# Kernel optimization log

Measured on AMD Instinct MI355X. Metric: run time of the kernel, lower is better.

The kernel has to match this reference:

```python
import jax, jax.numpy as jnp
import numpy as np

VOCAB = 32000
D_VEC = 1024

def setup_inputs() -> dict:
    key = jax.random.key(0)
    kq, ke = jax.random.split(key)
    q = jax.random.normal(kq, (4, 1024, D_VEC), dtype=jnp.float32)
    # emb_matrix ~ Uniform(-0.1, 0.1), as in torch .uniform_(-0.1, 0.1)
    emb_matrix = jax.random.uniform(ke, (VOCAB, D_VEC), dtype=jnp.float32,
                                    minval=-0.1, maxval=0.1)
    return {"q": q, "emb_matrix": emb_matrix}

def reference(q, emb_matrix):
    # scores: [B, L, V] = q @ emb^T  (unscaled single-head attention)
    scores = jnp.einsum('bld,vd->blv', q, emb_matrix)
    attn = jax.nn.softmax(scores, axis=-1)
    # dropout is identity in eval / deterministic reference
    ctx = jnp.einsum('blv,vd->bld', attn, emb_matrix)
    return ctx + q
```

## Files before the change

kernel.cpp:

```cpp
#include <hip/hip_runtime.h>
#include <hip/hip_bf16.h>

#define D_DIM 1024
#define VOCABSZ 32000
#define NROWSZ 4096
#define MBLK 64
#define LOG2E 1.44269504088896340736f

typedef unsigned short u16;
typedef short s8v __attribute__((ext_vector_type(8)));
typedef short s4v __attribute__((ext_vector_type(4)));
typedef float f4v __attribute__((ext_vector_type(4)));
typedef __attribute__((address_space(3))) const char* lds_p3;

static __device__ __forceinline__ u16 f2bf(float f) {
  union { float f; unsigned int u; } x; x.f = f;
  unsigned int r = x.u + 0x7fffu + ((x.u >> 16) & 1u);
  return (u16)(r >> 16);
}
static __device__ __forceinline__ unsigned int pack2(float lo, float hi) {
  return (unsigned int)f2bf(lo) | ((unsigned int)f2bf(hi) << 16);
}
static __device__ __forceinline__ unsigned int pk_rn(float lo, float hi) {
  float2 f; f.x = lo; f.y = hi;
  union { __hip_bfloat162 h; unsigned int u; } v;
  v.h = __float22bfloat162_rn(f);
  return v.u;
}
#define EXP2(x) __builtin_amdgcn_exp2f(x)

static __device__ __forceinline__ float bf2f(u16 b) {
  union { unsigned int u; float f; } x; x.u = ((unsigned int)b) << 16;
  return x.f;
}
static __device__ __forceinline__ float bfu_lo(unsigned int u) {
  union { unsigned int u; float f; } x; x.u = u << 16; return x.f;
}
static __device__ __forceinline__ float bfu_hi(unsigned int u) {
  union { unsigned int u; float f; } x; x.u = u & 0xffff0000u; return x.f;
}
static __device__ __forceinline__ f4v MFMA(s8v a, s8v b, f4v c) {
  return __builtin_amdgcn_mfma_f32_16x16x32_bf16(a, b, c, 0, 0, 0);
}

#define GLOAD_LDS16(gp, lp)                                                  \
  __builtin_amdgcn_global_load_lds(                                         \
      (const __attribute__((address_space(1))) void*)(gp),                  \
      (__attribute__((address_space(3))) void*)(lp), 16, 0, 0)

__global__ __launch_bounds__(256) void cvt3_kernel(const float* __restrict__ emb,
                                                   char* __restrict__ ETt) {
  const int b = blockIdx.x, t = threadIdx.x;
  const int v0 = b * 32;
  char* outp = ETt + ((size_t)b << 16);
#pragma unroll
  for (int k = 0; k < 16; ++k) {
    int ci = t + 256 * k;
    int v = ci >> 7;
    int d8 = ci & 127;
    const float* s = emb + (size_t)(v0 + v) * D_DIM + d8 * 8;
    float4 a = *(const float4*)s;
    float4 bb = *(const float4*)(s + 4);
    uint4 x;
    x.x = pack2(a.x, a.y); x.y = pack2(a.z, a.w);
    x.z = pack2(bb.x, bb.y); x.w = pack2(bb.z, bb.w);
    int off = ((v >> 2) * 64 + (d8 >> 1)) * 128 + (v & 3) * 32 + (d8 & 1) * 16;
    *(uint4*)(outp + off) = x;
  }
}

template <int NSPLIT>
__global__ __launch_bounds__(512, 2) void flash9_kernel(
    const float* __restrict__ qg, const char* __restrict__ ETt,
    float* __restrict__ out, u16* __restrict__ pctx, float* __restrict__ pstat) {
  __shared__ char ring[2 * 65536];
  __shared__ uint2 Sred[8 * 4 * 64];
  __shared__ char Plds[4096];
  __shared__ float lred[8][16];

  const int tid = threadIdx.x;
  const int w = tid >> 6;
  const int l = tid & 63;
  const int g = l >> 4;
  const int c = l & 15;
  const int ds = w & 3;
  const int mh = w >> 2;
  const int bid = blockIdx.x;
  const int sp = (NSPLIT == 4) ? (bid & 3) : 0;
  const int rb = (NSPLIT == 4) ? (bid >> 2) : bid;
  const int row0 = rb * MBLK;
  const int vslice = VOCABSZ / NSPLIT;
  const int ntiles = vslice / 32;
  const int gt0 = sp * ntiles;

  const f4v fzero = {0.f, 0.f, 0.f, 0.f};

  s8v qf[2][8];
#pragma unroll
  for (int mt = 0; mt < 2; ++mt)
#pragma unroll
    for (int kt = 0; kt < 8; ++kt) {
      const float* src = qg + (size_t)(row0 + mh * 32 + 16 * mt + c) * D_DIM +
                         ds * 256 + 32 * kt + 8 * g;
      float4 a = *(const float4*)src;
      float4 b = *(const float4*)(src + 4);
      s8v v;
      v[0] = (short)f2bf(a.x * LOG2E); v[1] = (short)f2bf(a.y * LOG2E);
      v[2] = (short)f2bf(a.z * LOG2E); v[3] = (short)f2bf(a.w * LOG2E);
      v[4] = (short)f2bf(b.x * LOG2E); v[5] = (short)f2bf(b.y * LOG2E);
      v[6] = (short)f2bf(b.z * LOG2E); v[7] = (short)f2bf(b.w * LOG2E);
      qf[mt][kt] = v;
    }

  f4v acc[2][16];
#pragma unroll
  for (int mt = 0; mt < 2; ++mt)
#pragma unroll
    for (int nt = 0; nt < 16; ++nt) acc[mt][nt] = fzero;

  float lcur = 0.f;

#define STAGE(U)                                                             \
  {                                                                          \
    const char* _gs = ETt + (((size_t)(gt0 + (U))) << 16) + tid * 16;        \
    char* _ls = ring + (((U) & 1) << 16) + tid * 16;                         \
    _Pragma("unroll") for (int _j = 0; _j < 8; ++_j)                         \
        GLOAD_LDS16(_gs + _j * 8192, _ls + _j * 8192);                       \
  }

  STAGE(0);
  __syncthreads();

  for (int t = 0; t < ntiles; ++t) {
    const char* buf = ring + ((t & 1) << 16);

#pragma unroll
    for (int vt = 0; vt < 2; ++vt) {
      const char* bp = buf + (((4 * vt + (c >> 2)) * 64 + 16 * ds + (g >> 1)) * 128 +
                              (c & 3) * 32 + (g & 1) * 16);
      f4v st0 = fzero, st1 = fzero;
#pragma unroll
      for (int kt = 0; kt < 8; ++kt) {
        s8v ek = *(const s8v*)(bp + kt * 256);
        st0 = MFMA(ek, qf[0][kt], st0);
        st1 = MFMA(ek, qf[1][kt], st1);
      }
      int qb = ((mh * 4 + vt * 2) * 4 + ds) * 64 + l;
      uint2 pk;
      pk.x = pk_rn(st0[0], st0[1]); pk.y = pk_rn(st0[2], st0[3]);
      Sred[qb] = pk;
      pk.x = pk_rn(st1[0], st1[1]); pk.y = pk_rn(st1[2], st1[3]);
      Sred[qb + 256] = pk;
    }
    __syncthreads();

    {
      int qq = mh * 4 + ds;
      f4v ss = fzero;
#pragma unroll
      for (int ww = 0; ww < 4; ++ww) {
        uint2 u = Sred[(qq * 4 + ww) * 64 + l];
        ss[0] += bfu_lo(u.x); ss[1] += bfu_hi(u.x);
        ss[2] += bfu_lo(u.y); ss[3] += bfu_hi(u.y);
      }
      float p0 = EXP2(ss[0]), p1 = EXP2(ss[1]);
      float p2 = EXP2(ss[2]), p3 = EXP2(ss[3]);
      int pb = mh * 2048 + (16 * (ds & 1) + c) * 64 + (16 * (ds >> 1) + 4 * g) * 2;
      uint2 pw; pw.x = pk_rn(p0, p1); pw.y = pk_rn(p2, p3);
      *(uint2*)(Plds + pb) = pw;
      lcur += (p0 + p1) + (p2 + p3);
    }
    __syncthreads();

    if (t + 1 < ntiles) STAGE(t + 1);

    {
      int pab = mh * 2048 + c * 64 + g * 16;
      s8v pa0 = *(const s8v*)(Plds + pab);
      s8v pa1 = *(const s8v*)(Plds + pab + 1024);
#pragma unroll
      for (int bb = 0; bb < 2; ++bb) {
        s4v trv[16];
#pragma unroll
        for (int k = 0; k < 8; ++k) {
          int nt = bb * 8 + k;
          const char* a0 = buf + ((2 * g) * 64 + 16 * ds + nt) * 128 + c * 2;
          asm volatile("ds_read_b64_tr_b16 %0, %1"
                       : "=v"(trv[2 * k]) : "v"((lds_p3)a0));
          asm volatile("ds_read_b64_tr_b16 %0, %1"
                       : "=v"(trv[2 * k + 1]) : "v"((lds_p3)(a0 + 8192)));
        }
        asm volatile("s_waitcnt lgkmcnt(0)" ::: "memory");
        __builtin_amdgcn_sched_barrier(0);
#pragma unroll
        for (int k = 0; k < 8; ++k) {
          int nt = bb * 8 + k;
          union { s4v s[2]; s8v v; } ev;
          ev.s[0] = trv[2 * k]; ev.s[1] = trv[2 * k + 1];
          acc[0][nt] = MFMA(pa0, ev.v, acc[0][nt]);
          acc[1][nt] = MFMA(pa1, ev.v, acc[1][nt]);
        }
      }
    }
  }
#undef STAGE

  {
    float lp = lcur;
    lp += __shfl_xor(lp, 16);
    lp += __shfl_xor(lp, 32);
    __syncthreads();
    if (g == 0) lred[mh * 4 + ds][c] = lp;
  }
  __syncthreads();

  if (NSPLIT == 1) {
#pragma unroll
    for (int mt = 0; mt < 2; ++mt) {
      float inv[4];
#pragma unroll
      for (int r = 0; r < 4; ++r)
        inv[r] = 1.f / (lred[mh * 4 + mt][4 * g + r] + lred[mh * 4 + 2 + mt][4 * g + r]);
#pragma unroll
      for (int nt = 0; nt < 16; ++nt)
#pragma unroll
        for (int r = 0; r < 4; ++r) {
          size_t o = (size_t)(row0 + mh * 32 + 16 * mt + 4 * g + r) * D_DIM +
                     ds * 256 + 16 * nt + c;
          out[o] = acc[mt][nt][r] * inv[r] + qg[o];
        }
    }
  } else {
    u16* pc = pctx + (size_t)sp * NROWSZ * D_DIM;
#pragma unroll
    for (int mt = 0; mt < 2; ++mt)
#pragma unroll
      for (int nt = 0; nt < 16; ++nt)
#pragma unroll
        for (int r = 0; r < 4; ++r)
          pc[(size_t)(row0 + mh * 32 + 16 * mt + 4 * g + r) * D_DIM +
             ds * 256 + 16 * nt + c] = f2bf(acc[mt][nt][r]);
    if (ds < 2 && g == 0)
      pstat[(size_t)sp * NROWSZ + row0 + mh * 32 + 16 * ds + c] =
          lred[mh * 4 + ds][c] + lred[mh * 4 + 2 + ds][c];
  }
}

__global__ __launch_bounds__(256) void combine2_kernel(const float* __restrict__ qg,
                                                       const u16* __restrict__ pctx,
                                                       const float* __restrict__ pstat,
                                                       float* __restrict__ out) {
  const int r = blockIdx.x;
  const int t = threadIdx.x;
  float L = pstat[r] + pstat[NROWSZ + r] + pstat[2 * NROWSZ + r] + pstat[3 * NROWSZ + r];
  float inv = 1.f / L;
  size_t o = (size_t)r * D_DIM + t * 4;
  float sx = 0.f, sy = 0.f, sz = 0.f, sw = 0.f;
#pragma unroll
  for (int sp = 0; sp < 4; ++sp) {
    ushort4 u = *(const ushort4*)(pctx + (size_t)sp * NROWSZ * D_DIM + o);
    sx += bf2f(u.x); sy += bf2f(u.y); sz += bf2f(u.z); sw += bf2f(u.w);
  }
  float4 qv = *(const float4*)(qg + o);
  float4 res;
  res.x = sx * inv + qv.x;
  res.y = sy * inv + qv.y;
  res.z = sz * inv + qv.z;
  res.w = sw * inv + qv.w;
  *(float4*)(out + o) = res;
}

__global__ __launch_bounds__(256) void naive_kernel(const float* __restrict__ qg,
                                                    const float* __restrict__ emb,
                                                    float* __restrict__ out) {
  __shared__ float s[VOCABSZ];
  __shared__ float qrow[D_DIM];
  __shared__ float lsh[4];
  const int r = blockIdx.x;
  const int t = threadIdx.x;
  for (int i = t; i < D_DIM; i += 256) qrow[i] = qg[(size_t)r * D_DIM + i];
  __syncthreads();
  float lpart = 0.f;
  for (int v = t; v < VOCABSZ; v += 256) {
    float dot = 0.f;
    for (int d = 0; d < D_DIM; d += 4) {
      float4 e = *(const float4*)(emb + (size_t)v * D_DIM + d);
      dot += qrow[d] * e.x + qrow[d + 1] * e.y + qrow[d + 2] * e.z + qrow[d + 3] * e.w;
    }
    float p = exp2f(dot * LOG2E);
    s[v] = p;
    lpart += p;
  }
  for (int o = 32; o; o >>= 1) lpart += __shfl_xor(lpart, o);
  if ((t & 63) == 0) lsh[t >> 6] = lpart;
  __syncthreads();
  float inv = 1.f / (lsh[0] + lsh[1] + lsh[2] + lsh[3]);
  float ax = 0.f, ay = 0.f, az = 0.f, aw = 0.f;
  for (int v = 0; v < VOCABSZ; ++v) {
    float p = s[v];
    float4 e = *(const float4*)(emb + (size_t)v * D_DIM + t * 4);
    ax += p * e.x; ay += p * e.y; az += p * e.z; aw += p * e.w;
  }
  size_t o = (size_t)r * D_DIM + t * 4;
  float4 qv = *(const float4*)(qg + o);
  float4 res;
  res.x = ax * inv + qv.x;
  res.y = ay * inv + qv.y;
  res.z = az * inv + qv.z;
  res.w = aw * inv + qv.w;
  *(float4*)(out + o) = res;
}

extern "C" void kernel_launch(void* const* d_in, const int* in_sizes, int n_in,
                              void* d_out, int out_size, void* d_ws, size_t ws_size,
                              hipStream_t stream) {
  const float* q = (const float*)d_in[0];
  const float* emb = (const float*)d_in[1];
  float* out = (float*)d_out;
  char* ws = (char*)d_ws;

  const size_t ETT_BYTES = 65536000ull;
  const size_t PCTX_BYTES = 4ull * NROWSZ * D_DIM * 2;
  const size_t PSTAT_BYTES = 4ull * NROWSZ * 4;

  if (ws_size >= ETT_BYTES + PCTX_BYTES + PSTAT_BYTES) {
    char* ETt = ws;
    u16* pctx = (u16*)(ws + ETT_BYTES);
    float* pstat = (float*)(ws + ETT_BYTES + PCTX_BYTES);
    cvt3_kernel<<<VOCABSZ / 32, 256, 0, stream>>>(emb, ETt);
    flash9_kernel<4><<<256, 512, 0, stream>>>(q, ETt, out, pctx, pstat);
    combine2_kernel<<<NROWSZ, 256, 0, stream>>>(q, pctx, pstat, out);
  } else if (ws_size >= ETT_BYTES) {
    char* ETt = ws;
    cvt3_kernel<<<VOCABSZ / 32, 256, 0, stream>>>(emb, ETt);
    flash9_kernel<1><<<NROWSZ / MBLK, 512, 0, stream>>>(q, ETt, out, nullptr, nullptr);
  } else {
    naive_kernel<<<NROWSZ, 256, 0, stream>>>(q, emb, out);
  }
}
```

Baseline: 591.0 us.

## Software-pipeline the P·V MFMAs across tiles to overlap them with the softmax exp phase

Splits each tile's P·V accumulation into four quarters. The first two quarters run right after the tile's probabilities are ready. The last two are deferred into the next iteration's softmax phase, where they are interleaved with the Sred reduction and exp2 work and issued at raised wave priority. The P buffer in LDS is double-buffered so the previous tile's probabilities stay readable, and a drain block after the loop finishes the final tile's deferred MFMAs. The goal is to hide the exp/reduction latency behind matrix work, at the cost of extra LDS, more register pressure from live transposed fragments, and more complex control flow.

```diff
diff --git a/kernel.cpp b/kernel.cpp
--- a/kernel.cpp
+++ b/kernel.cpp
@@ -42,6 +42,12 @@
 static __device__ __forceinline__ f4v MFMA(s8v a, s8v b, f4v c) {
   return __builtin_amdgcn_mfma_f32_16x16x32_bf16(a, b, c, 0, 0, 0);
 }
+
+#define LGKM0_SB()                                            \
+  do {                                                        \
+    asm volatile("s_waitcnt lgkmcnt(0)" ::: "memory");        \
+    __builtin_amdgcn_sched_barrier(0);                        \
+  } while (0)
 
 #define GLOAD_LDS16(gp, lp)                                                  \
   __builtin_amdgcn_global_load_lds(                                         \
@@ -70,12 +76,12 @@
 }
 
 template <int NSPLIT>
-__global__ __launch_bounds__(512, 2) void flash9_kernel(
+__global__ __launch_bounds__(512, 2) void flash11_kernel(
     const float* __restrict__ qg, const char* __restrict__ ETt,
     float* __restrict__ out, u16* __restrict__ pctx, float* __restrict__ pstat) {
   __shared__ char ring[2 * 65536];
   __shared__ uint2 Sred[8 * 4 * 64];
-  __shared__ char Plds[4096];
+  __shared__ char Plds[2 * 4096];
   __shared__ float lred[8][16];
 
   const int tid = threadIdx.x;
@@ -119,6 +125,8 @@
     for (int nt = 0; nt < 16; ++nt) acc[mt][nt] = fzero;
 
   float lcur = 0.f;
+  const int pab_s = mh * 2048 + c * 64 + g * 16;
+  const int abase_s = ((2 * g) * 64 + 16 * ds) * 128 + c * 2;
 
 #define STAGE(U)                                                             \
   {                                                                          \
@@ -128,11 +136,29 @@
         GLOAD_LDS16(_gs + _j * 8192, _ls + _j * 8192);                       \
   }
 
+#define TR4(arr, NTB, ABASE)                                                 \
+  _Pragma("unroll") for (int _k = 0; _k < 4; ++_k) {                         \
+    const char* _a0 = (ABASE) + ((NTB) + _k) * 128;                          \
+    asm volatile("ds_read_b64_tr_b16 %0, %1"                                 \
+                 : "=v"(arr[2 * _k]) : "v"((lds_p3)_a0));                    \
+    asm volatile("ds_read_b64_tr_b16 %0, %1"                                 \
+                 : "=v"(arr[2 * _k + 1]) : "v"((lds_p3)(_a0 + 8192)));       \
+  }
+
+#define MF4(arr, NTB, PA0, PA1)                                              \
+  _Pragma("unroll") for (int _k = 0; _k < 4; ++_k) {                         \
+    union { s4v s[2]; s8v v; } _ev;                                          \
+    _ev.s[0] = arr[2 * _k]; _ev.s[1] = arr[2 * _k + 1];                      \
+    acc[0][(NTB) + _k] = MFMA((PA0), _ev.v, acc[0][(NTB) + _k]);             \
+    acc[1][(NTB) + _k] = MFMA((PA1), _ev.v, acc[1][(NTB) + _k]);             \
+  }
+
   STAGE(0);
-  __syncthreads();
 
   for (int t = 0; t < ntiles; ++t) {
     const char* buf = ring + ((t & 1) << 16);
+
+    __syncthreads();
 
 #pragma unroll
     for (int vt = 0; vt < 2; ++vt) {
@@ -155,55 +181,93 @@
     __syncthreads();
 
     {
-      int qq = mh * 4 + ds;
-      f4v ss = fzero;
-#pragma unroll
-      for (int ww = 0; ww < 4; ++ww) {
-        uint2 u = Sred[(qq * 4 + ww) * 64 + l];
-        ss[0] += bfu_lo(u.x); ss[1] += bfu_hi(u.x);
-        ss[2] += bfu_lo(u.y); ss[3] += bfu_hi(u.y);
+      const int qq = mh * 4 + ds;
+      if (t > 0) {
+        const char* bufp = ring + (((t - 1) & 1) << 16);
+        const char* abp = bufp + abase_s;
+        const char* Pp = Plds + (((t - 1) & 1) << 12);
+        s8v p0p = *(const s8v*)(Pp + pab_s);
+        s8v p1p = *(const s8v*)(Pp + pab_s + 1024);
+        s4v tv[8];
+        TR4(tv, 8, abp);
+        f4v ss = fzero;
+#pragma unroll
+        for (int ww = 0; ww < 4; ++ww) {
+          uint2 u = Sred[(qq * 4 + ww) * 64 + l];
+          ss[0] += bfu_lo(u.x); ss[1] += bfu_hi(u.x);
+          ss[2] += bfu_lo(u.y); ss[3] += bfu_hi(u.y);
+        }
+        LGKM0_SB();
+        __builtin_amdgcn_s_setprio(1);
+        MF4(tv, 8, p0p, p1p);
+        __builtin_amdgcn_s_setprio(0);
+        TR4(tv, 12, abp);
+        {
+          float p0 = EXP2(ss[0]), p1 = EXP2(ss[1]);
+          float p2 = EXP2(ss[2]), p3 = EXP2(ss[3]);
+          int pb = ((t & 1) << 12) + mh * 2048 +
+                   (16 * (ds & 1) + c) * 64 + (16 * (ds >> 1) + 4 * g) * 2;
+          uint2 pw; pw.x = pk_rn(p0, p1); pw.y = pk_rn(p2, p3);
+          *(uint2*)(Plds + pb) = pw;
+          lcur += (p0 + p1) + (p2 + p3);
+        }
+        LGKM0_SB();
+        __builtin_amdgcn_s_setprio(1);
+        MF4(tv, 12, p0p, p1p);
+        __builtin_amdgcn_s_setprio(0);
+      } else {
+        f4v ss = fzero;
+#pragma unroll
+        for (int ww = 0; ww < 4; ++ww) {
+          uint2 u = Sred[(qq * 4 + ww) * 64 + l];
+          ss[0] += bfu_lo(u.x); ss[1] += bfu_hi(u.x);
+          ss[2] += bfu_lo(u.y); ss[3] += bfu_hi(u.y);
+        }
+        float p0 = EXP2(ss[0]), p1 = EXP2(ss[1]);
+        float p2 = EXP2(ss[2]), p3 = EXP2(ss[3]);
+        int pb = ((t & 1) << 12) + mh * 2048 +
+                 (16 * (ds & 1) + c) * 64 + (16 * (ds >> 1) + 4 * g) * 2;
+        uint2 pw; pw.x = pk_rn(p0, p1); pw.y = pk_rn(p2, p3);
+        *(uint2*)(Plds + pb) = pw;
+        lcur += (p0 + p1) + (p2 + p3);
       }
-      float p0 = EXP2(ss[0]), p1 = EXP2(ss[1]);
-      float p2 = EXP2(ss[2]), p3 = EXP2(ss[3]);
-      int pb = mh * 2048 + (16 * (ds & 1) + c) * 64 + (16 * (ds >> 1) + 4 * g) * 2;
-      uint2 pw; pw.x = pk_rn(p0, p1); pw.y = pk_rn(p2, p3);
-      *(uint2*)(Plds + pb) = pw;
-      lcur += (p0 + p1) + (p2 + p3);
     }
     __syncthreads();
 
     if (t + 1 < ntiles) STAGE(t + 1);
 
     {
-      int pab = mh * 2048 + c * 64 + g * 16;
-      s8v pa0 = *(const s8v*)(Plds + pab);
-      s8v pa1 = *(const s8v*)(Plds + pab + 1024);
-#pragma unroll
-      for (int bb = 0; bb < 2; ++bb) {
-        s4v trv[16];
-#pragma unroll
-        for (int k = 0; k < 8; ++k) {
-          int nt = bb * 8 + k;
-          const char* a0 = buf + ((2 * g) * 64 + 16 * ds + nt) * 128 + c * 2;
-          asm volatile("ds_read_b64_tr_b16 %0, %1"
-                       : "=v"(trv[2 * k]) : "v"((lds_p3)a0));
-          asm volatile("ds_read_b64_tr_b16 %0, %1"
-                       : "=v"(trv[2 * k + 1]) : "v"((lds_p3)(a0 + 8192)));
-        }
-        asm volatile("s_waitcnt lgkmcnt(0)" ::: "memory");
-        __builtin_amdgcn_sched_barrier(0);
-#pragma unroll
-        for (int k = 0; k < 8; ++k) {
-          int nt = bb * 8 + k;
-          union { s4v s[2]; s8v v; } ev;
-          ev.s[0] = trv[2 * k]; ev.s[1] = trv[2 * k + 1];
-          acc[0][nt] = MFMA(pa0, ev.v, acc[0][nt]);
-          acc[1][nt] = MFMA(pa1, ev.v, acc[1][nt]);
-        }
-      }
-    }
+      const char* Pc = Plds + ((t & 1) << 12);
+      s8v p0 = *(const s8v*)(Pc + pab_s);
+      s8v p1 = *(const s8v*)(Pc + pab_s + 1024);
+      const char* ab = buf + abase_s;
+      s4v tv[8];
+      TR4(tv, 0, ab);
+      LGKM0_SB();
+      MF4(tv, 0, p0, p1);
+      TR4(tv, 4, ab);
+      LGKM0_SB();
+      MF4(tv, 4, p0, p1);
+    }
+  }
+  {
+    const int tl = ntiles - 1;
+    const char* bufp = ring + ((tl & 1) << 16);
+    const char* abp = bufp + abase_s;
+    const char* Pp = Plds + ((tl & 1) << 12);
+    s8v p0p = *(const s8v*)(Pp + pab_s);
+    s8v p1p = *(const s8v*)(Pp + pab_s + 1024);
+    s4v tv[8];
+    TR4(tv, 8, abp);
+    LGKM0_SB();
+    MF4(tv, 8, p0p, p1p);
+    TR4(tv, 12, abp);
+    LGKM0_SB();
+    MF4(tv, 12, p0p, p1p);
   }
 #undef STAGE
+#undef TR4
+#undef MF4
 
   {
     float lp = lcur;
@@ -328,12 +392,12 @@
     u16* pctx = (u16*)(ws + ETT_BYTES);
     float* pstat = (float*)(ws + ETT_BYTES + PCTX_BYTES);
     cvt3_kernel<<<VOCABSZ / 32, 256, 0, stream>>>(emb, ETt);
-    flash9_kernel<4><<<256, 512, 0, stream>>>(q, ETt, out, pctx, pstat);
+    flash11_kernel<4><<<256, 512, 0, stream>>>(q, ETt, out, pctx, pstat);
     combine2_kernel<<<NROWSZ, 256, 0, stream>>>(q, pctx, pstat, out);
   } else if (ws_size >= ETT_BYTES) {
     char* ETt = ws;
     cvt3_kernel<<<VOCABSZ / 32, 256, 0, stream>>>(emb, ETt);
-    flash9_kernel<1><<<NROWSZ / MBLK, 512, 0, stream>>>(q, ETt, out, nullptr, nullptr);
+    flash11_kernel<1><<<NROWSZ / MBLK, 512, 0, stream>>>(q, ETt, out, nullptr, nullptr);
   } else {
     naive_kernel<<<NROWSZ, 256, 0, stream>>>(q, emb, out);
   }
```

After: 633.4 us. +7.2%, slower.

## Stagger warp halves so QK, softmax and PV phases overlap across row groups

Applied to the files above, without the earlier changes.

Splits the 8 waves into two row-halves that run the QK, softmax and PV phases out of phase with each other. While half 0 computes QK scores, half 1 runs PV on the previous tile, and the other phases interleave the same way. The goal is to overlap MFMA-heavy phases with the exp/reduction phase, so matrix units stay busy across the barriers. In exchange it adds an extra barrier per tile and a tail PV step. Half 1 also reads the previous ring buffer, so correctness depends on the staging order and barriers leaving that buffer intact.

```diff
diff --git a/kernel.cpp b/kernel.cpp
--- a/kernel.cpp
+++ b/kernel.cpp
@@ -70,7 +70,7 @@
 }
 
 template <int NSPLIT>
-__global__ __launch_bounds__(512, 2) void flash9_kernel(
+__global__ __launch_bounds__(512, 2) void flash14_kernel(
     const float* __restrict__ qg, const char* __restrict__ ETt,
     float* __restrict__ out, u16* __restrict__ pctx, float* __restrict__ pstat) {
   __shared__ char ring[2 * 65536];
@@ -119,6 +119,8 @@
     for (int nt = 0; nt < 16; ++nt) acc[mt][nt] = fzero;
 
   float lcur = 0.f;
+  const int pab_s = mh * 2048 + c * 64 + g * 16;
+  const int abase_s = ((2 * g) * 64 + 16 * ds) * 128 + c * 2;
 
 #define STAGE(U)                                                             \
   {                                                                          \
@@ -128,82 +130,111 @@
         GLOAD_LDS16(_gs + _j * 8192, _ls + _j * 8192);                       \
   }
 
+#define QK_STEP(BUF)                                                         \
+  {                                                                          \
+    _Pragma("unroll") for (int vt = 0; vt < 2; ++vt) {                       \
+      const char* bp = (BUF) +                                               \
+          (((4 * vt + (c >> 2)) * 64 + 16 * ds + (g >> 1)) * 128 +           \
+           (c & 3) * 32 + (g & 1) * 16);                                     \
+      f4v st0 = fzero, st1 = fzero;                                          \
+      _Pragma("unroll") for (int kt = 0; kt < 8; ++kt) {                     \
+        s8v ek = *(const s8v*)(bp + kt * 256);                               \
+        st0 = MFMA(ek, qf[0][kt], st0);                                      \
+        st1 = MFMA(ek, qf[1][kt], st1);                                      \
+      }                                                                      \
+      int qb = ((mh * 4 + vt * 2) * 4 + ds) * 64 + l;                        \
+      uint2 pk;                                                              \
+      pk.x = pk_rn(st0[0], st0[1]); pk.y = pk_rn(st0[2], st0[3]);            \
+      Sred[qb] = pk;                                                         \
+      pk.x = pk_rn(st1[0], st1[1]); pk.y = pk_rn(st1[2], st1[3]);            \
+      Sred[qb + 256] = pk;                                                   \
+    }                                                                        \
+  }
+
+#define SM_STEP()                                                            \
+  {                                                                          \
+    int qq = mh * 4 + ds;                                                    \
+    f4v ss = fzero;                                                          \
+    _Pragma("unroll") for (int ww = 0; ww < 4; ++ww) {                       \
+      uint2 u = Sred[(qq * 4 + ww) * 64 + l];                                \
+      ss[0] += bfu_lo(u.x); ss[1] += bfu_hi(u.x);                            \
+      ss[2] += bfu_lo(u.y); ss[3] += bfu_hi(u.y);                            \
+    }                                                                        \
+    float p0 = EXP2(ss[0]), p1 = EXP2(ss[1]);                                \
+    float p2 = EXP2(ss[2]), p3 = EXP2(ss[3]);                                \
+    int pb = mh * 2048 + (16 * (ds & 1) + c) * 64 +                          \
+             (16 * (ds >> 1) + 4 * g) * 2;                                   \
+    uint2 pw; pw.x = pk_rn(p0, p1); pw.y = pk_rn(p2, p3);                    \
+    *(uint2*)(Plds + pb) = pw;                                               \
+    lcur += (p0 + p1) + (p2 + p3);                                           \
+  }
+
+#define PV_STEP(BUF)                                                         \
+  {                                                                          \
+    s8v pa0 = *(const s8v*)(Plds + pab_s);                                   \
+    s8v pa1 = *(const s8v*)(Plds + pab_s + 1024);                            \
+    const char* ab = (BUF) + abase_s;                                        \
+    _Pragma("unroll") for (int bb = 0; bb < 2; ++bb) {                       \
+      s4v trv[16];                                                           \
+      _Pragma("unroll") for (int k = 0; k < 8; ++k) {                        \
+        int nt = bb * 8 + k;                                                 \
+        const char* a0 = ab + nt * 128;                                      \
+        asm volatile("ds_read_b64_tr_b16 %0, %1"                             \
+                     : "=v"(trv[2 * k]) : "v"((lds_p3)a0));                  \
+        asm volatile("ds_read_b64_tr_b16 %0, %1"                             \
+                     : "=v"(trv[2 * k + 1]) : "v"((lds_p3)(a0 + 8192)));     \
+      }                                                                      \
+      asm volatile("s_waitcnt lgkmcnt(0)" ::: "memory");                     \
+      __builtin_amdgcn_sched_barrier(0);                                     \
+      _Pragma("unroll") for (int k = 0; k < 8; ++k) {                        \
+        int nt = bb * 8 + k;                                                 \
+        union { s4v s[2]; s8v v; } ev;                                       \
+        ev.s[0] = trv[2 * k]; ev.s[1] = trv[2 * k + 1];                      \
+        acc[0][nt] = MFMA(pa0, ev.v, acc[0][nt]);                            \
+        acc[1][nt] = MFMA(pa1, ev.v, acc[1][nt]);                            \
+      }                                                                      \
+    }                                                                        \
+  }
+
   STAGE(0);
-  __syncthreads();
 
   for (int t = 0; t < ntiles; ++t) {
     const char* buf = ring + ((t & 1) << 16);
-
-#pragma unroll
-    for (int vt = 0; vt < 2; ++vt) {
-      const char* bp = buf + (((4 * vt + (c >> 2)) * 64 + 16 * ds + (g >> 1)) * 128 +
-                              (c & 3) * 32 + (g & 1) * 16);
-      f4v st0 = fzero, st1 = fzero;
-#pragma unroll
-      for (int kt = 0; kt < 8; ++kt) {
-        s8v ek = *(const s8v*)(bp + kt * 256);
-        st0 = MFMA(ek, qf[0][kt], st0);
-        st1 = MFMA(ek, qf[1][kt], st1);
-      }
-      int qb = ((mh * 4 + vt * 2) * 4 + ds) * 64 + l;
-      uint2 pk;
-      pk.x = pk_rn(st0[0], st0[1]); pk.y = pk_rn(st0[2], st0[3]);
-      Sred[qb] = pk;
-      pk.x = pk_rn(st1[0], st1[1]); pk.y = pk_rn(st1[2], st1[3]);
-      Sred[qb + 256] = pk;
-    }
+    const char* bufp = ring + (((t - 1) & 1) << 16);
+
     __syncthreads();
 
-    {
-      int qq = mh * 4 + ds;
-      f4v ss = fzero;
-#pragma unroll
-      for (int ww = 0; ww < 4; ++ww) {
-        uint2 u = Sred[(qq * 4 + ww) * 64 + l];
-        ss[0] += bfu_lo(u.x); ss[1] += bfu_hi(u.x);
-        ss[2] += bfu_lo(u.y); ss[3] += bfu_hi(u.y);
-      }
-      float p0 = EXP2(ss[0]), p1 = EXP2(ss[1]);
-      float p2 = EXP2(ss[2]), p3 = EXP2(ss[3]);
-      int pb = mh * 2048 + (16 * (ds & 1) + c) * 64 + (16 * (ds >> 1) + 4 * g) * 2;
-      uint2 pw; pw.x = pk_rn(p0, p1); pw.y = pk_rn(p2, p3);
-      *(uint2*)(Plds + pb) = pw;
-      lcur += (p0 + p1) + (p2 + p3);
+    if (mh == 0) {
+      QK_STEP(buf);
+    } else if (t > 0) {
+      PV_STEP(bufp);
     }
     __syncthreads();
 
+    if (mh == 0) {
+      SM_STEP();
+    } else {
+      QK_STEP(buf);
+    }
+    __syncthreads();
+
     if (t + 1 < ntiles) STAGE(t + 1);
 
-    {
-      int pab = mh * 2048 + c * 64 + g * 16;
-      s8v pa0 = *(const s8v*)(Plds + pab);
-      s8v pa1 = *(const s8v*)(Plds + pab + 1024);
-#pragma unroll
-      for (int bb = 0; bb < 2; ++bb) {
-        s4v trv[16];
-#pragma unroll
-        for (int k = 0; k < 8; ++k) {
-          int nt = bb * 8 + k;
-          const char* a0 = buf + ((2 * g) * 64 + 16 * ds + nt) * 128 + c * 2;
-          asm volatile("ds_read_b64_tr_b16 %0, %1"
-                       : "=v"(trv[2 * k]) : "v"((lds_p3)a0));
-          asm volatile("ds_read_b64_tr_b16 %0, %1"
-                       : "=v"(trv[2 * k + 1]) : "v"((lds_p3)(a0 + 8192)));
-        }
-        asm volatile("s_waitcnt lgkmcnt(0)" ::: "memory");
-        __builtin_amdgcn_sched_barrier(0);
-#pragma unroll
-        for (int k = 0; k < 8; ++k) {
-          int nt = bb * 8 + k;
-          union { s4v s[2]; s8v v; } ev;
-          ev.s[0] = trv[2 * k]; ev.s[1] = trv[2 * k + 1];
-          acc[0][nt] = MFMA(pa0, ev.v, acc[0][nt]);
-          acc[1][nt] = MFMA(pa1, ev.v, acc[1][nt]);
-        }
-      }
-    }
+    if (mh == 0) {
+      PV_STEP(buf);
+    } else {
+      SM_STEP();
+    }
+  }
+  __syncthreads();
+  if (mh == 1) {
+    const char* bufl = ring + (((ntiles - 1) & 1) << 16);
+    PV_STEP(bufl);
   }
 #undef STAGE
+#undef QK_STEP
+#undef SM_STEP
+#undef PV_STEP
 
   {
     float lp = lcur;
@@ -328,12 +359,12 @@
     u16* pctx = (u16*)(ws + ETT_BYTES);
     float* pstat = (float*)(ws + ETT_BYTES + PCTX_BYTES);
     cvt3_kernel<<<VOCABSZ / 32, 256, 0, stream>>>(emb, ETt);
-    flash9_kernel<4><<<256, 512, 0, stream>>>(q, ETt, out, pctx, pstat);
+    flash14_kernel<4><<<256, 512, 0, stream>>>(q, ETt, out, pctx, pstat);
     combine2_kernel<<<NROWSZ, 256, 0, stream>>>(q, pctx, pstat, out);
   } else if (ws_size >= ETT_BYTES) {
     char* ETt = ws;
     cvt3_kernel<<<VOCABSZ / 32, 256, 0, stream>>>(emb, ETt);
-    flash9_kernel<1><<<NROWSZ / MBLK, 512, 0, stream>>>(q, ETt, out, nullptr, nullptr);
+    flash14_kernel<1><<<NROWSZ / MBLK, 512, 0, stream>>>(q, ETt, out, nullptr, nullptr);
   } else {
     naive_kernel<<<NROWSZ, 256, 0, stream>>>(q, emb, out);
   }
```

New measurement: 618.3 us. 4.6% more time.

## Shrink flash block to 32 rows with 4 waves and a single-buffered LDS tile

Applied to the files above, without the earlier changes.

Each workgroup now handles 32 query rows with 256 threads instead of 64 rows with 512, so the grid doubles to 512 blocks. The double-buffered 128 KB LDS ring becomes a single 64 KB buffer. The next tile is loaded only after the PV MFMAs finish, behind an extra barrier. The smaller LDS footprint and block size are meant to fit more blocks per CU and fill more of the GPU. In exchange, the global-to-LDS load no longer overlaps compute, and the embedding tiles are streamed twice as many times overall.

```diff
diff --git a/kernel.cpp b/kernel.cpp
--- a/kernel.cpp
+++ b/kernel.cpp
@@ -4,7 +4,7 @@
 #define D_DIM 1024
 #define VOCABSZ 32000
 #define NROWSZ 4096
-#define MBLK 64
+#define MBLK 32
 #define LOG2E 1.44269504088896340736f
 
 typedef unsigned short u16;
@@ -70,21 +70,20 @@
 }
 
 template <int NSPLIT>
-__global__ __launch_bounds__(512, 2) void flash9_kernel(
+__global__ __launch_bounds__(256, 2) void flash16_kernel(
     const float* __restrict__ qg, const char* __restrict__ ETt,
     float* __restrict__ out, u16* __restrict__ pctx, float* __restrict__ pstat) {
-  __shared__ char ring[2 * 65536];
-  __shared__ uint2 Sred[8 * 4 * 64];
-  __shared__ char Plds[4096];
-  __shared__ float lred[8][16];
+  __shared__ char ring[65536];
+  __shared__ uint2 Sred[4 * 4 * 64];
+  __shared__ char Plds[2048];
+  __shared__ float lred[4][16];
 
   const int tid = threadIdx.x;
   const int w = tid >> 6;
   const int l = tid & 63;
   const int g = l >> 4;
   const int c = l & 15;
-  const int ds = w & 3;
-  const int mh = w >> 2;
+  const int ds = w;
   const int bid = blockIdx.x;
   const int sp = (NSPLIT == 4) ? (bid & 3) : 0;
   const int rb = (NSPLIT == 4) ? (bid >> 2) : bid;
@@ -100,7 +99,7 @@
   for (int mt = 0; mt < 2; ++mt)
 #pragma unroll
     for (int kt = 0; kt < 8; ++kt) {
-      const float* src = qg + (size_t)(row0 + mh * 32 + 16 * mt + c) * D_DIM +
+      const float* src = qg + (size_t)(row0 + 16 * mt + c) * D_DIM +
                          ds * 256 + 32 * kt + 8 * g;
       float4 a = *(const float4*)src;
       float4 b = *(const float4*)(src + 4);
@@ -123,16 +122,17 @@
 #define STAGE(U)                                                             \
   {                                                                          \
     const char* _gs = ETt + (((size_t)(gt0 + (U))) << 16) + tid * 16;        \
-    char* _ls = ring + (((U) & 1) << 16) + tid * 16;                         \
-    _Pragma("unroll") for (int _j = 0; _j < 8; ++_j)                         \
-        GLOAD_LDS16(_gs + _j * 8192, _ls + _j * 8192);                       \
+    char* _ls = ring + tid * 16;                                             \
+    _Pragma("unroll") for (int _j = 0; _j < 16; ++_j)                        \
+        GLOAD_LDS16(_gs + _j * 4096, _ls + _j * 4096);                       \
   }
 
   STAGE(0);
-  __syncthreads();
 
   for (int t = 0; t < ntiles; ++t) {
-    const char* buf = ring + ((t & 1) << 16);
+    const char* buf = ring;
+
+    __syncthreads();
 
 #pragma unroll
     for (int vt = 0; vt < 2; ++vt) {
@@ -145,7 +145,7 @@
         st0 = MFMA(ek, qf[0][kt], st0);
         st1 = MFMA(ek, qf[1][kt], st1);
       }
-      int qb = ((mh * 4 + vt * 2) * 4 + ds) * 64 + l;
+      int qb = ((vt * 2) * 4 + ds) * 64 + l;
       uint2 pk;
       pk.x = pk_rn(st0[0], st0[1]); pk.y = pk_rn(st0[2], st0[3]);
       Sred[qb] = pk;
@@ -155,27 +155,24 @@
     __syncthreads();
 
     {
-      int qq = mh * 4 + ds;
       f4v ss = fzero;
 #pragma unroll
       for (int ww = 0; ww < 4; ++ww) {
-        uint2 u = Sred[(qq * 4 + ww) * 64 + l];
+        uint2 u = Sred[(ds * 4 + ww) * 64 + l];
         ss[0] += bfu_lo(u.x); ss[1] += bfu_hi(u.x);
         ss[2] += bfu_lo(u.y); ss[3] += bfu_hi(u.y);
       }
       float p0 = EXP2(ss[0]), p1 = EXP2(ss[1]);
       float p2 = EXP2(ss[2]), p3 = EXP2(ss[3]);
-      int pb = mh * 2048 + (16 * (ds & 1) + c) * 64 + (16 * (ds >> 1) + 4 * g) * 2;
+      int pb = (16 * (ds & 1) + c) * 64 + (16 * (ds >> 1) + 4 * g) * 2;
       uint2 pw; pw.x = pk_rn(p0, p1); pw.y = pk_rn(p2, p3);
       *(uint2*)(Plds + pb) = pw;
       lcur += (p0 + p1) + (p2 + p3);
     }
     __syncthreads();
 
-    if (t + 1 < ntiles) STAGE(t + 1);
-
     {
-      int pab = mh * 2048 + c * 64 + g * 16;
+      int pab = c * 64 + g * 16;
       s8v pa0 = *(const s8v*)(Plds + pab);
       s8v pa1 = *(const s8v*)(Plds + pab + 1024);
 #pragma unroll
@@ -202,6 +199,9 @@
         }
       }
     }
+    __syncthreads();
+
+    if (t + 1 < ntiles) STAGE(t + 1);
   }
 #undef STAGE
 
@@ -210,7 +210,7 @@
     lp += __shfl_xor(lp, 16);
     lp += __shfl_xor(lp, 32);
     __syncthreads();
-    if (g == 0) lred[mh * 4 + ds][c] = lp;
+    if (g == 0) lred[ds][c] = lp;
   }
   __syncthreads();
 
@@ -220,12 +220,12 @@
       float inv[4];
 #pragma unroll
       for (int r = 0; r < 4; ++r)
-        inv[r] = 1.f / (lred[mh * 4 + mt][4 * g + r] + lred[mh * 4 + 2 + mt][4 * g + r]);
+        inv[r] = 1.f / (lred[mt][4 * g + r] + lred[2 + mt][4 * g + r]);
 #pragma unroll
       for (int nt = 0; nt < 16; ++nt)
 #pragma unroll
         for (int r = 0; r < 4; ++r) {
-          size_t o = (size_t)(row0 + mh * 32 + 16 * mt + 4 * g + r) * D_DIM +
+          size_t o = (size_t)(row0 + 16 * mt + 4 * g + r) * D_DIM +
                      ds * 256 + 16 * nt + c;
           out[o] = acc[mt][nt][r] * inv[r] + qg[o];
         }
@@ -238,11 +238,11 @@
       for (int nt = 0; nt < 16; ++nt)
 #pragma unroll
         for (int r = 0; r < 4; ++r)
-          pc[(size_t)(row0 + mh * 32 + 16 * mt + 4 * g + r) * D_DIM +
+          pc[(size_t)(row0 + 16 * mt + 4 * g + r) * D_DIM +
              ds * 256 + 16 * nt + c] = f2bf(acc[mt][nt][r]);
     if (ds < 2 && g == 0)
-      pstat[(size_t)sp * NROWSZ + row0 + mh * 32 + 16 * ds + c] =
-          lred[mh * 4 + ds][c] + lred[mh * 4 + 2 + ds][c];
+      pstat[(size_t)sp * NROWSZ + row0 + 16 * ds + c] =
+          lred[ds][c] + lred[2 + ds][c];
   }
 }
 
@@ -328,12 +328,12 @@
     u16* pctx = (u16*)(ws + ETT_BYTES);
     float* pstat = (float*)(ws + ETT_BYTES + PCTX_BYTES);
     cvt3_kernel<<<VOCABSZ / 32, 256, 0, stream>>>(emb, ETt);
-    flash9_kernel<4><<<256, 512, 0, stream>>>(q, ETt, out, pctx, pstat);
+    flash16_kernel<4><<<(NROWSZ / MBLK) * 4, 256, 0, stream>>>(q, ETt, out, pctx, pstat);
     combine2_kernel<<<NROWSZ, 256, 0, stream>>>(q, pctx, pstat, out);
   } else if (ws_size >= ETT_BYTES) {
     char* ETt = ws;
     cvt3_kernel<<<VOCABSZ / 32, 256, 0, stream>>>(emb, ETt);
-    flash9_kernel<1><<<NROWSZ / MBLK, 512, 0, stream>>>(q, ETt, out, nullptr, nullptr);
+    flash16_kernel<1><<<NROWSZ / MBLK, 256, 0, stream>>>(q, ETt, out, nullptr, nullptr);
   } else {
     naive_kernel<<<NROWSZ, 256, 0, stream>>>(q, emb, out);
   }
```

Result: slower. 715.7 us (+21.1%).
